# Performance work log

Hardware: AMD Instinct MI355X
Metric: run time of the kernel (lower is better)

## Reference

```python
import jax, jax.numpy as jnp
import numpy as np

WH, WW = 7, 7
N = WH * WW
DIM = 128
NH = 4
HD = DIM // NH
B_IMG, NW = 64, 64
B_ = B_IMG * NW

def _relative_position_index():
    ch = np.arange(WH)
    cw = np.arange(WW)
    coords = np.stack(np.meshgrid(ch, cw, indexing='ij'))  # (2, Wh, Ww)
    coords = coords.reshape(2, -1)  # (2, N)
    rel = coords[:, :, None] - coords[:, None, :]  # (2, N, N)
    rel = rel.transpose(1, 2, 0)  # (N, N, 2)
    rel[:, :, 0] += WH - 1
    rel[:, :, 1] += WW - 1
    rel[:, :, 0] *= 2 * WW - 1
    return jnp.asarray(rel.sum(-1), dtype=jnp.int32)  # (N, N)

REL_IDX = _relative_position_index()

def setup_inputs() -> dict:
    key = jax.random.key(0)
    k1, k2, k3, k4, k5 = jax.random.split(key, 5)
    return {
        'x': jax.random.normal(k1, (B_, N, DIM), dtype=jnp.float32),
        'mask': jax.random.normal(k2, (NW, N, N), dtype=jnp.float32),
        'qkv_w': jax.random.normal(k3, (3 * DIM, DIM), dtype=jnp.float32) * 0.02,
        'qkv_b': jax.random.normal(k4, (3 * DIM,), dtype=jnp.float32) * 0.02,
        'rel_table': jax.random.normal(k5, ((2 * WH - 1) * (2 * WW - 1), NH), dtype=jnp.float32) * 0.02,
    }

def reference(x, mask, qkv_w, qkv_b, rel_table):
    B_tot, n, c = x.shape
    scale = HD ** (-0.5)
    # qkv projection; torch split order is (nH, hD, qkv) innermost-to-outermost
    qkv = x @ qkv_w.T + qkv_b                      # (B_, N, 3C)
    qkv = qkv.reshape(B_tot, n, NH, HD, 3)
    q = jnp.transpose(qkv[..., 0], (0, 2, 1, 3))   # (B_, nH, N, hD)
    k = jnp.transpose(qkv[..., 1], (0, 2, 1, 3))
    v = jnp.transpose(qkv[..., 2], (0, 2, 1, 3))
    attn = jnp.einsum('bhnd,bhmd->bhnm', q, k) * scale  # (B_, nH, N, N)
    bias = jnp.transpose(rel_table[REL_IDX.reshape(-1)].reshape(n, n, NH), (2, 0, 1))
    attn = attn + bias[None]
    nW = mask.shape[0]
    attn = attn.reshape(B_tot // nW, nW, NH, n, n) + mask[None, :, None]
    attn = attn.reshape(B_tot, NH, n, n)
    attn = jax.nn.softmax(attn, axis=-1)
    out = jnp.einsum('bhnm,bhmd->bhnd', attn, v)   # (B_, nH, N, hD)
    return jnp.transpose(out, (0, 2, 1, 3)).reshape(B_tot, n, c)
```

## Files before the change

### kernel.cpp

```cpp
#include <hip/hip_runtime.h>


typedef short bf16x8 __attribute__((ext_vector_type(8)));
typedef float f32x4 __attribute__((ext_vector_type(4)));

#define DEVI __device__ __forceinline__

DEVI unsigned short f2b(float f) {
    unsigned u = __builtin_bit_cast(unsigned, f);
    u += 0x7fffu + ((u >> 16) & 1u);
    return (unsigned short)(u >> 16);
}

#define WS_BIAS_OFF 98304
#define WS_COMB_OFF 131072
#define WS_NEED     (131072u + 64u * 4u * 2401u * 4u)

__global__ void prep_kernel(const float* __restrict__ qkvw, const float* __restrict__ qkvb,
                            const float* __restrict__ maskg, const float* __restrict__ relt,
                            unsigned short* __restrict__ wb, float* __restrict__ bb,
                            float* __restrict__ comb) {
    const int blk = blockIdx.x;
    const int tid = threadIdx.x;
    if (blk < 384) {
        const int s = blk >> 7, r7 = blk & 127, h = r7 >> 5, d = r7 & 31;
        const int c = h * 96 + d * 3 + s;
        const float mul = (s == 0) ? 0.17677669529663687f : 1.0f;
        if (tid < 128) wb[blk * 128 + tid] = f2b(qkvw[c * 128 + tid] * mul);
        if (tid == 128) bb[blk] = qkvb[c] * mul;
    } else {
        const int wh = blk - 384;
        const int w = wh >> 2, h = wh & 3;
        const float* mw = maskg + w * 2401;
        float* cbp = comb + wh * 2401;
        for (int i = tid; i < 2401; i += 256) {
            int n = i / 49, m = i - n * 49;
            int md = m / 7, mm = m - md * 7;
            int nd = n / 7, nm = n - nd * 7;
            int ridx = (md - nd + 6) * 13 + (mm - nm + 6);
            cbp[i] = mw[m * 49 + n] + relt[ridx * 4 + h];
        }
    }
}

struct __align__(16) Smem {
    unsigned short qk[2][4][64][32];
    union {
        unsigned short xs[64][136];
        unsigned short vt[4][32][72];
    } b;
};

template <bool USE_WS>
__global__ __launch_bounds__(512, 6) void wattn_kernel(
    const float* __restrict__ xg, const unsigned short* __restrict__ wb,
    const float* __restrict__ bb, const float* __restrict__ comb,
    const float* __restrict__ maskg, const float* __restrict__ qkvw,
    const float* __restrict__ qkvb, const float* __restrict__ relt,
    float* __restrict__ outg)
{
    __shared__ Smem sm;
    const int tid  = threadIdx.x;
    const int lane = tid & 63;
    const int wv   = tid >> 6;
    const int h    = wv & 3;
    const int half = wv >> 2;
    const int lr   = lane & 15;
    const int lq   = lane >> 4;
    const int bI   = blockIdx.x;

    const float* xb = xg + (size_t)bI * 6272;
    #pragma unroll
    for (int it = 0; it < 4; ++it) {
        int i = it * 512 + tid;
        if (i < 1568) {
            float4 v = ((const float4*)xb)[i];
            int row = i >> 5, col = (i & 31) << 2;
            *(ushort4*)&sm.b.xs[row][col] =
                make_ushort4(f2b(v.x), f2b(v.y), f2b(v.z), f2b(v.w));
        }
    }
    if (tid < 480) {
        int idx = tid << 2;
        *(ushort4*)&sm.b.xs[49 + (idx >> 7)][idx & 127] = make_ushort4(0, 0, 0, 0);
    }
    __syncthreads();

    bf16x8 af[4][2];
    #pragma unroll
    for (int ks = 0; ks < 4; ++ks)
        #pragma unroll
        for (int mtl = 0; mtl < 2; ++mtl)
            af[ks][mtl] = *(const bf16x8*)&sm.b.xs[(half * 2 + mtl) * 16 + lr][ks * 32 + lq * 8];
    __syncthreads();

    if constexpr (USE_WS) {
        #pragma unroll
        for (int j = 0; j < 6; ++j) {
            const int s     = j >> 1;
            const int dhalf = j & 1;
            const int cp    = s * 128 + h * 32 + dhalf * 16 + lr;
            const int dd    = dhalf * 16 + lr;
            const float bc  = bb[cp];
            f32x4 acc[2];
            acc[0] = f32x4{0.f, 0.f, 0.f, 0.f};
            acc[1] = f32x4{0.f, 0.f, 0.f, 0.f};
            #pragma unroll
            for (int ks = 0; ks < 4; ++ks) {
                bf16x8 bf = *(const bf16x8*)&wb[cp * 128 + ks * 32 + lq * 8];
                #pragma unroll
                for (int mtl = 0; mtl < 2; ++mtl)
                    acc[mtl] = __builtin_amdgcn_mfma_f32_16x16x32_bf16(af[ks][mtl], bf, acc[mtl], 0, 0, 0);
            }
            #pragma unroll
            for (int mtl = 0; mtl < 2; ++mtl) {
                const int m0 = (half * 2 + mtl) * 16 + lq * 4;
                if (s == 2) {
                    *(ushort4*)&sm.b.vt[h][dd][m0] =
                        make_ushort4(f2b(acc[mtl][0] + bc), f2b(acc[mtl][1] + bc),
                                     f2b(acc[mtl][2] + bc), f2b(acc[mtl][3] + bc));
                } else {
                    #pragma unroll
                    for (int r = 0; r < 4; ++r)
                        sm.qk[s][h][m0 + r][dd] = f2b(acc[mtl][r] + bc);
                }
            }
        }
    } else {
        unsigned short* sbase = (unsigned short*)&sm;
        #pragma unroll
        for (int j = 0; j < 6; ++j) {
            const int c = (h * 6 + j) * 16 + lr;
            const float bc = qkvb[c];
            const int rem = j * 16 + lr;
            const int dd = rem / 3, s = rem % 3;
            const float mulv = (s == 0) ? 0.17677669529663687f : 1.0f;
            f32x4 acc[2];
            acc[0] = f32x4{0.f, 0.f, 0.f, 0.f};
            acc[1] = f32x4{0.f, 0.f, 0.f, 0.f};
            #pragma unroll
            for (int ks = 0; ks < 4; ++ks) {
                const float4* wp = (const float4*)(qkvw + c * 128 + ks * 32 + lq * 8);
                float4 w0 = wp[0], w1 = wp[1];
                bf16x8 t;
                t[0] = (short)f2b(w0.x); t[1] = (short)f2b(w0.y);
                t[2] = (short)f2b(w0.z); t[3] = (short)f2b(w0.w);
                t[4] = (short)f2b(w1.x); t[5] = (short)f2b(w1.y);
                t[6] = (short)f2b(w1.z); t[7] = (short)f2b(w1.w);
                #pragma unroll
                for (int mtl = 0; mtl < 2; ++mtl)
                    acc[mtl] = __builtin_amdgcn_mfma_f32_16x16x32_bf16(af[ks][mtl], t, acc[mtl], 0, 0, 0);
            }
            #pragma unroll
            for (int mtl = 0; mtl < 2; ++mtl)
                #pragma unroll
                for (int r = 0; r < 4; ++r) {
                    int m = (half * 2 + mtl) * 16 + lq * 4 + r;
                    int soff = (s == 2) ? (16384 + (h * 32 + dd) * 72 + m)
                                        : (s * 8192 + h * 2048 + m * 32 + dd);
                    sbase[soff] = f2b((acc[mtl][r] + bc) * mulv);
                }
        }
    }
    __syncthreads();

    bf16x8 kf[4];
    #pragma unroll
    for (int t = 0; t < 4; ++t)
        kf[t] = *(const bf16x8*)&sm.qk[1][h][t * 16 + lr][lq * 8];

    const float* cwh = comb + (size_t)((bI & 63) * 4 + h) * 2401;
    const float* mw  = maskg + (size_t)(bI & 63) * 2401;
    float* ob = outg + (size_t)bI * 6272;
    const int src0 = ((lq & 1) * 2) * 16 + lr;
    const int src1 = src0 + 16;
    const bool up  = (lq >= 2);

    #pragma unroll
    for (int bl = 0; bl < 2; ++bl) {
        const int mt = half * 2 + bl;
        const int m  = mt * 16 + lr;
        const int mi = m < 48 ? m : 48;

        f32x4 st[4];
        if constexpr (USE_WS) {
            f32x4 cc[4];
            #pragma unroll
            for (int a = 0; a < 4; ++a)
                #pragma unroll
                for (int r = 0; r < 4; ++r) {
                    int n = a * 16 + lq * 4 + r;
                    cc[a][r] = (n < 49) ? cwh[n * 49 + mi] : -1e30f;
                }
            bf16x8 qf = *(const bf16x8*)&sm.qk[0][h][m][lq * 8];
            #pragma unroll
            for (int a = 0; a < 4; ++a)
                st[a] = __builtin_amdgcn_mfma_f32_16x16x32_bf16(kf[a], qf, cc[a], 0, 0, 0);
        } else {
            bf16x8 qf = *(const bf16x8*)&sm.qk[0][h][m][lq * 8];
            #pragma unroll
            for (int a = 0; a < 4; ++a) {
                f32x4 z = f32x4{0.f, 0.f, 0.f, 0.f};
                st[a] = __builtin_amdgcn_mfma_f32_16x16x32_bf16(kf[a], qf, z, 0, 0, 0);
            }
            const int md = mi / 7, mm = mi - md * 7;
            #pragma unroll
            for (int a = 0; a < 4; ++a)
                #pragma unroll
                for (int r = 0; r < 4; ++r) {
                    int n = a * 16 + lq * 4 + r;
                    int ni = n < 48 ? n : 48;
                    int nd = ni / 7, nm = ni - nd * 7;
                    int ridx = (md - nd + 6) * 13 + (mm - nm + 6);
                    float v = st[a][r] + relt[ridx * 4 + h] + mw[mi * 49 + ni];
                    st[a][r] = (n < 49) ? v : -1e30f;
                }
        }

        float mx = -3.4e38f;
        #pragma unroll
        for (int a = 0; a < 4; ++a)
            #pragma unroll
            for (int r = 0; r < 4; ++r) mx = fmaxf(mx, st[a][r]);
        mx = fmaxf(mx, __shfl_xor(mx, 16));
        mx = fmaxf(mx, __shfl_xor(mx, 32));
        float sum = 0.f;
        #pragma unroll
        for (int a = 0; a < 4; ++a)
            #pragma unroll
            for (int r = 0; r < 4; ++r) {
                float e = __expf(st[a][r] - mx);
                st[a][r] = e;
                sum += e;
            }
        sum += __shfl_xor(sum, 16);
        sum += __shfl_xor(sum, 32);
        const float inv = 1.f / sum;

        unsigned pk[4][2];
        #pragma unroll
        for (int a = 0; a < 4; ++a) {
            pk[a][0] = (unsigned)f2b(st[a][0] * inv) | ((unsigned)f2b(st[a][1] * inv) << 16);
            pk[a][1] = (unsigned)f2b(st[a][2] * inv) | ((unsigned)f2b(st[a][3] * inv) << 16);
        }

        f32x4 o[2];
        o[0] = f32x4{0.f, 0.f, 0.f, 0.f};
        o[1] = f32x4{0.f, 0.f, 0.f, 0.f};
        #pragma unroll
        for (int kt = 0; kt < 2; ++kt) {
            unsigned ea0 = (unsigned)__shfl((int)pk[2 * kt][0], src0);
            unsigned ea1 = (unsigned)__shfl((int)pk[2 * kt][1], src0);
            unsigned ea2 = (unsigned)__shfl((int)pk[2 * kt][0], src1);
            unsigned ea3 = (unsigned)__shfl((int)pk[2 * kt][1], src1);
            unsigned eb0 = (unsigned)__shfl((int)pk[2 * kt + 1][0], src0);
            unsigned eb1 = (unsigned)__shfl((int)pk[2 * kt + 1][1], src0);
            unsigned eb2 = (unsigned)__shfl((int)pk[2 * kt + 1][0], src1);
            unsigned eb3 = (unsigned)__shfl((int)pk[2 * kt + 1][1], src1);
            union { unsigned u[4]; bf16x8 v; } pu;
            pu.u[0] = up ? eb0 : ea0;
            pu.u[1] = up ? eb1 : ea1;
            pu.u[2] = up ? eb2 : ea2;
            pu.u[3] = up ? eb3 : ea3;
            #pragma unroll
            for (int dt = 0; dt < 2; ++dt) {
                bf16x8 vf = *(const bf16x8*)&sm.b.vt[h][dt * 16 + lr][kt * 32 + lq * 8];
                o[dt] = __builtin_amdgcn_mfma_f32_16x16x32_bf16(vf, pu.v, o[dt], 0, 0, 0);
            }
        }

        if (m < 49) {
            #pragma unroll
            for (int dt = 0; dt < 2; ++dt) {
                float4 v = make_float4(o[dt][0], o[dt][1], o[dt][2], o[dt][3]);
                *(float4*)&ob[m * 128 + h * 32 + dt * 16 + lq * 4] = v;
            }
        }
    }
}

extern "C" void kernel_launch(void* const* d_in, const int* in_sizes, int n_in,
                              void* d_out, int out_size, void* d_ws, size_t ws_size,
                              hipStream_t stream) {
    const float* x    = (const float*)d_in[0];
    const float* mask = (const float*)d_in[1];
    const float* qkvw = (const float*)d_in[2];
    const float* qkvb = (const float*)d_in[3];
    const float* relt = (const float*)d_in[4];
    float* out = (float*)d_out;

    if (d_ws != nullptr && ws_size >= (size_t)WS_NEED) {
        unsigned short* wbf = (unsigned short*)d_ws;
        float* bbf  = (float*)((char*)d_ws + WS_BIAS_OFF);
        float* comb = (float*)((char*)d_ws + WS_COMB_OFF);
        prep_kernel<<<640, 256, 0, stream>>>(qkvw, qkvb, mask, relt, wbf, bbf, comb);
        wattn_kernel<true><<<4096, 512, 0, stream>>>(x, wbf, bbf, comb, mask, qkvw, qkvb, relt, out);
    } else {
        wattn_kernel<false><<<4096, 512, 0, stream>>>(x, nullptr, nullptr, nullptr, mask, qkvw, qkvb, relt, out);
    }
}
```

Measured before the change: 269.3 us.

## Pad combined bias/mask table to 64-wide rows and vectorize loads, reorganize Q/K smem

```diff
diff --git a/kernel.cpp b/kernel.cpp
--- a/kernel.cpp
+++ b/kernel.cpp
@@ -12,39 +12,55 @@
     return (unsigned short)(u >> 16);
 }
 
+DEVI unsigned pack2(float lo, float hi) {
+    return (unsigned)f2b(lo) | ((unsigned)f2b(hi) << 16);
+}
+
 #define WS_BIAS_OFF 98304
 #define WS_COMB_OFF 131072
-#define WS_NEED     (131072u + 64u * 4u * 2401u * 4u)
-
-__global__ void prep_kernel(const float* __restrict__ qkvw, const float* __restrict__ qkvb,
-                            const float* __restrict__ maskg, const float* __restrict__ relt,
-                            unsigned short* __restrict__ wb, float* __restrict__ bb,
-                            float* __restrict__ comb) {
-    const int blk = blockIdx.x;
-    const int tid = threadIdx.x;
-    if (blk < 384) {
-        const int s = blk >> 7, r7 = blk & 127, h = r7 >> 5, d = r7 & 31;
-        const int c = h * 96 + d * 3 + s;
+#define COMB_ELEMS  802816u
+#define WS_NEED     (131072u + COMB_ELEMS * 4u)
+
+__global__ __launch_bounds__(256) void prep_kernel(
+    const float* __restrict__ qkvw, const float* __restrict__ qkvb,
+    const float* __restrict__ maskg, const float* __restrict__ relt,
+    unsigned short* __restrict__ wb, float* __restrict__ bb,
+    float* __restrict__ comb)
+{
+    const int g = blockIdx.x * 256 + threadIdx.x;
+    if (g < 49152) {
+        const int row = g >> 7, col = g & 127;
+        const int s = row >> 7, r7 = row & 127, hh = r7 >> 5, d = r7 & 31;
+        const int c = hh * 96 + d * 3 + s;
         const float mul = (s == 0) ? 0.17677669529663687f : 1.0f;
-        if (tid < 128) wb[blk * 128 + tid] = f2b(qkvw[c * 128 + tid] * mul);
-        if (tid == 128) bb[blk] = qkvb[c] * mul;
+        wb[row * 128 + col] = f2b(qkvw[c * 128 + col] * mul);
+    } else if (g < 49536) {
+        const int row = g - 49152;
+        const int s = row >> 7, r7 = row & 127, hh = r7 >> 5, d = r7 & 31;
+        const int c = hh * 96 + d * 3 + s;
+        const float mul = (s == 0) ? 0.17677669529663687f : 1.0f;
+        bb[row] = qkvb[c] * mul;
     } else {
-        const int wh = blk - 384;
-        const int w = wh >> 2, h = wh & 3;
-        const float* mw = maskg + w * 2401;
-        float* cbp = comb + wh * 2401;
-        for (int i = tid; i < 2401; i += 256) {
-            int n = i / 49, m = i - n * 49;
-            int md = m / 7, mm = m - md * 7;
-            int nd = n / 7, nm = n - nd * 7;
-            int ridx = (md - nd + 6) * 13 + (mm - nm + 6);
-            cbp[i] = mw[m * 49 + n] + relt[ridx * 4 + h];
+        const unsigned g2 = (unsigned)(g - 49536);
+        if (g2 < COMB_ELEMS) {
+            const int wh = g2 / 3136;
+            const int rr = g2 - wh * 3136;
+            const int m = rr >> 6, n = rr & 63;
+            const int w = wh >> 2, hh = wh & 3;
+            float v = -1e30f;
+            if (n < 49) {
+                const int md = m / 7, mm = m - md * 7;
+                const int nd = n / 7, nm = n - nd * 7;
+                const int ridx = (md - nd + 6) * 13 + (mm - nm + 6);
+                v = maskg[w * 2401 + m * 49 + n] + relt[ridx * 4 + hh];
+            }
+            comb[g2] = v;
         }
     }
 }
 
 struct __align__(16) Smem {
-    unsigned short qk[2][4][64][32];
+    unsigned short qk[2][4][4][64][8];
     union {
         unsigned short xs[64][136];
         unsigned short vt[4][32][72];
@@ -76,8 +92,7 @@
         if (i < 1568) {
             float4 v = ((const float4*)xb)[i];
             int row = i >> 5, col = (i & 31) << 2;
-            *(ushort4*)&sm.b.xs[row][col] =
-                make_ushort4(f2b(v.x), f2b(v.y), f2b(v.z), f2b(v.w));
+            *(uint2*)&sm.b.xs[row][col] = make_uint2(pack2(v.x, v.y), pack2(v.z, v.w));
         }
     }
     if (tid < 480) {
@@ -95,46 +110,63 @@
     __syncthreads();
 
     if constexpr (USE_WS) {
+        bf16x8 wcur[4];
+        {
+            const int cp0 = h * 32 + lr;
+            #pragma unroll
+            for (int ks = 0; ks < 4; ++ks)
+                wcur[ks] = *(const bf16x8*)&wb[cp0 * 128 + ks * 32 + lq * 8];
+        }
         #pragma unroll
         for (int j = 0; j < 6; ++j) {
-            const int s     = j >> 1;
-            const int dhalf = j & 1;
-            const int cp    = s * 128 + h * 32 + dhalf * 16 + lr;
-            const int dd    = dhalf * 16 + lr;
-            const float bc  = bb[cp];
+            const int s = j >> 1, dh = j & 1;
+            const int dd = dh * 16 + lr;
+            const int cp = s * 128 + h * 32 + dd;
+            const float bc = bb[cp];
+            bf16x8 wnxt[4];
+            if (j < 5) {
+                const int jn = j + 1;
+                const int cpn = (jn >> 1) * 128 + h * 32 + (jn & 1) * 16 + lr;
+                #pragma unroll
+                for (int ks = 0; ks < 4; ++ks)
+                    wnxt[ks] = *(const bf16x8*)&wb[cpn * 128 + ks * 32 + lq * 8];
+            }
             f32x4 acc[2];
             acc[0] = f32x4{0.f, 0.f, 0.f, 0.f};
             acc[1] = f32x4{0.f, 0.f, 0.f, 0.f};
             #pragma unroll
-            for (int ks = 0; ks < 4; ++ks) {
-                bf16x8 bf = *(const bf16x8*)&wb[cp * 128 + ks * 32 + lq * 8];
+            for (int ks = 0; ks < 4; ++ks)
                 #pragma unroll
                 for (int mtl = 0; mtl < 2; ++mtl)
-                    acc[mtl] = __builtin_amdgcn_mfma_f32_16x16x32_bf16(af[ks][mtl], bf, acc[mtl], 0, 0, 0);
-            }
+                    acc[mtl] = __builtin_amdgcn_mfma_f32_16x16x32_bf16(af[ks][mtl], wcur[ks], acc[mtl], 0, 0, 0);
             #pragma unroll
             for (int mtl = 0; mtl < 2; ++mtl) {
                 const int m0 = (half * 2 + mtl) * 16 + lq * 4;
+                const unsigned p01 = pack2(acc[mtl][0] + bc, acc[mtl][1] + bc);
+                const unsigned p23 = pack2(acc[mtl][2] + bc, acc[mtl][3] + bc);
                 if (s == 2) {
-                    *(ushort4*)&sm.b.vt[h][dd][m0] =
-                        make_ushort4(f2b(acc[mtl][0] + bc), f2b(acc[mtl][1] + bc),
-                                     f2b(acc[mtl][2] + bc), f2b(acc[mtl][3] + bc));
+                    *(uint2*)&sm.b.vt[h][dd][m0] = make_uint2(p01, p23);
                 } else {
-                    #pragma unroll
-                    for (int r = 0; r < 4; ++r)
-                        sm.qk[s][h][m0 + r][dd] = f2b(acc[mtl][r] + bc);
+                    unsigned short* qp = &sm.qk[s][h][dh * 2 + (lr >> 3)][m0][lr & 7];
+                    qp[0]  = (unsigned short)p01;
+                    qp[8]  = (unsigned short)(p01 >> 16);
+                    qp[16] = (unsigned short)p23;
+                    qp[24] = (unsigned short)(p23 >> 16);
                 }
             }
+            if (j < 5) {
+                #pragma unroll
+                for (int ks = 0; ks < 4; ++ks) wcur[ks] = wnxt[ks];
+            }
         }
     } else {
-        unsigned short* sbase = (unsigned short*)&sm;
         #pragma unroll
         for (int j = 0; j < 6; ++j) {
-            const int c = (h * 6 + j) * 16 + lr;
-            const float bc = qkvb[c];
-            const int rem = j * 16 + lr;
-            const int dd = rem / 3, s = rem % 3;
-            const float mulv = (s == 0) ? 0.17677669529663687f : 1.0f;
+            const int s = j >> 1, dh = j & 1;
+            const int dd = dh * 16 + lr;
+            const int c = h * 96 + dd * 3 + s;
+            const float mul = (s == 0) ? 0.17677669529663687f : 1.0f;
+            const float bc = qkvb[c] * mul;
             f32x4 acc[2];
             acc[0] = f32x4{0.f, 0.f, 0.f, 0.f};
             acc[1] = f32x4{0.f, 0.f, 0.f, 0.f};
@@ -142,35 +174,51 @@
             for (int ks = 0; ks < 4; ++ks) {
                 const float4* wp = (const float4*)(qkvw + c * 128 + ks * 32 + lq * 8);
                 float4 w0 = wp[0], w1 = wp[1];
-                bf16x8 t;
-                t[0] = (short)f2b(w0.x); t[1] = (short)f2b(w0.y);
-                t[2] = (short)f2b(w0.z); t[3] = (short)f2b(w0.w);
-                t[4] = (short)f2b(w1.x); t[5] = (short)f2b(w1.y);
-                t[6] = (short)f2b(w1.z); t[7] = (short)f2b(w1.w);
+                union { unsigned u[4]; bf16x8 v; } tw;
+                tw.u[0] = pack2(w0.x * mul, w0.y * mul);
+                tw.u[1] = pack2(w0.z * mul, w0.w * mul);
+                tw.u[2] = pack2(w1.x * mul, w1.y * mul);
+                tw.u[3] = pack2(w1.z * mul, w1.w * mul);
                 #pragma unroll
                 for (int mtl = 0; mtl < 2; ++mtl)
-                    acc[mtl] = __builtin_amdgcn_mfma_f32_16x16x32_bf16(af[ks][mtl], t, acc[mtl], 0, 0, 0);
-            }
-            #pragma unroll
-            for (int mtl = 0; mtl < 2; ++mtl)
-                #pragma unroll
-                for (int r = 0; r < 4; ++r) {
-                    int m = (half * 2 + mtl) * 16 + lq * 4 + r;
-                    int soff = (s == 2) ? (16384 + (h * 32 + dd) * 72 + m)
-                                        : (s * 8192 + h * 2048 + m * 32 + dd);
-                    sbase[soff] = f2b((acc[mtl][r] + bc) * mulv);
+                    acc[mtl] = __builtin_amdgcn_mfma_f32_16x16x32_bf16(af[ks][mtl], tw.v, acc[mtl], 0, 0, 0);
+            }
+            #pragma unroll
+            for (int mtl = 0; mtl < 2; ++mtl) {
+                const int m0 = (half * 2 + mtl) * 16 + lq * 4;
+                const unsigned p01 = pack2(acc[mtl][0] + bc, acc[mtl][1] + bc);
+                const unsigned p23 = pack2(acc[mtl][2] + bc, acc[mtl][3] + bc);
+                if (s == 2) {
+                    *(uint2*)&sm.b.vt[h][dd][m0] = make_uint2(p01, p23);
+                } else {
+                    unsigned short* qp = &sm.qk[s][h][dh * 2 + (lr >> 3)][m0][lr & 7];
+                    qp[0]  = (unsigned short)p01;
+                    qp[8]  = (unsigned short)(p01 >> 16);
+                    qp[16] = (unsigned short)p23;
+                    qp[24] = (unsigned short)(p23 >> 16);
                 }
-        }
+            }
+        }
+    }
+
+    const float* cwh = comb + (size_t)((bI & 63) * 4 + h) * 3136;
+    const float* mw  = maskg + (size_t)(bI & 63) * 2401;
+    f32x4 cc0[4];
+    if constexpr (USE_WS) {
+        const int m0b = (half * 2) * 16 + lr;
+        const int mi0 = m0b < 48 ? m0b : 48;
+        const float* cr = cwh + mi0 * 64;
+        #pragma unroll
+        for (int a = 0; a < 4; ++a)
+            cc0[a] = *(const f32x4*)&cr[a * 16 + lq * 4];
     }
     __syncthreads();
 
     bf16x8 kf[4];
     #pragma unroll
     for (int t = 0; t < 4; ++t)
-        kf[t] = *(const bf16x8*)&sm.qk[1][h][t * 16 + lr][lq * 8];
-
-    const float* cwh = comb + (size_t)((bI & 63) * 4 + h) * 2401;
-    const float* mw  = maskg + (size_t)(bI & 63) * 2401;
+        kf[t] = *(const bf16x8*)&sm.qk[1][h][lq][t * 16 + lr][0];
+
     float* ob = outg + (size_t)bI * 6272;
     const int src0 = ((lq & 1) * 2) * 16 + lr;
     const int src1 = src0 + 16;
@@ -183,21 +231,22 @@
         const int mi = m < 48 ? m : 48;
 
         f32x4 st[4];
+        bf16x8 qf = *(const bf16x8*)&sm.qk[0][h][lq][m][0];
         if constexpr (USE_WS) {
             f32x4 cc[4];
-            #pragma unroll
-            for (int a = 0; a < 4; ++a)
-                #pragma unroll
-                for (int r = 0; r < 4; ++r) {
-                    int n = a * 16 + lq * 4 + r;
-                    cc[a][r] = (n < 49) ? cwh[n * 49 + mi] : -1e30f;
-                }
-            bf16x8 qf = *(const bf16x8*)&sm.qk[0][h][m][lq * 8];
+            if (bl == 0) {
+                #pragma unroll
+                for (int a = 0; a < 4; ++a) cc[a] = cc0[a];
+            } else {
+                const float* cr = cwh + mi * 64;
+                #pragma unroll
+                for (int a = 0; a < 4; ++a)
+                    cc[a] = *(const f32x4*)&cr[a * 16 + lq * 4];
+            }
             #pragma unroll
             for (int a = 0; a < 4; ++a)
                 st[a] = __builtin_amdgcn_mfma_f32_16x16x32_bf16(kf[a], qf, cc[a], 0, 0, 0);
         } else {
-            bf16x8 qf = *(const bf16x8*)&sm.qk[0][h][m][lq * 8];
             #pragma unroll
             for (int a = 0; a < 4; ++a) {
                 f32x4 z = f32x4{0.f, 0.f, 0.f, 0.f};
@@ -240,8 +289,8 @@
         unsigned pk[4][2];
         #pragma unroll
         for (int a = 0; a < 4; ++a) {
-            pk[a][0] = (unsigned)f2b(st[a][0] * inv) | ((unsigned)f2b(st[a][1] * inv) << 16);
-            pk[a][1] = (unsigned)f2b(st[a][2] * inv) | ((unsigned)f2b(st[a][3] * inv) << 16);
+            pk[a][0] = pack2(st[a][0] * inv, st[a][1] * inv);
+            pk[a][1] = pack2(st[a][2] * inv, st[a][3] * inv);
         }
 
         f32x4 o[2];
@@ -293,7 +342,7 @@
         unsigned short* wbf = (unsigned short*)d_ws;
         float* bbf  = (float*)((char*)d_ws + WS_BIAS_OFF);
         float* comb = (float*)((char*)d_ws + WS_COMB_OFF);
-        prep_kernel<<<640, 256, 0, stream>>>(qkvw, qkvb, mask, relt, wbf, bbf, comb);
+        prep_kernel<<<3330, 256, 0, stream>>>(qkvw, qkvb, mask, relt, wbf, bbf, comb);
         wattn_kernel<true><<<4096, 512, 0, stream>>>(x, wbf, bbf, comb, mask, qkvw, qkvb, relt, out);
     } else {
         wattn_kernel<false><<<4096, 512, 0, stream>>>(x, nullptr, nullptr, nullptr, mask, qkvw, qkvb, relt, out);
```

New measurement: 365.3 us. +35.6%, slower.
